# Optimization experiments

Measured on AMD Instinct MI355X. Metric: run time of the kernel, lower is better.

Reference implementation:

```python
import jax, jax.numpy as jnp
import numpy as np

N = 50000
E = 800000
G = 8
IN, HID, OUT = 128, 256, 128
BN_EPS = 1e-5


def _linear_params(key, fan_in, fan_out):
    k1, k2 = jax.random.split(key)
    s = 1.0 / np.sqrt(fan_in)
    w = jax.random.uniform(k1, (fan_out, fan_in), jnp.float32, -s, s)
    b = jax.random.uniform(k2, (fan_out,), jnp.float32, -s, s)
    return w, b


def setup_inputs() -> dict:
    key = jax.random.key(0)
    ks = jax.random.split(key, 16)
    inp = {
        "x": jax.random.normal(ks[0], (N, IN), jnp.float32),
        "src": jax.random.randint(ks[1], (E,), 0, N, jnp.int32),
        "dst": jax.random.randint(ks[2], (E,), 0, N, jnp.int32),
        "graph_ids": jnp.sort(jax.random.randint(ks[3], (N,), 0, G, jnp.int32)),
    }
    dims = [(IN, HID, HID), (HID, HID, HID), (HID, OUT, OUT)]
    for i, (d_in, d_mid, d_out) in enumerate(dims):
        kk = jax.random.split(ks[4 + i], 2)
        w1, b1 = _linear_params(kk[0], d_in, d_mid)
        w2, b2 = _linear_params(kk[1], d_mid, d_out)
        inp[f"w1_{i}"] = w1
        inp[f"b1_{i}"] = b1
        inp[f"w2_{i}"] = w2
        inp[f"b2_{i}"] = b2
        inp[f"eps_{i}"] = jnp.zeros((), jnp.float32)          # learn_eps, init 0
        inp[f"gamma_{i}"] = jnp.ones((d_out,), jnp.float32)   # BatchNorm weight
        inp[f"beta_{i}"] = jnp.zeros((d_out,), jnp.float32)   # BatchNorm bias
    return inp


def _gin_layer(h, src, dst, w1, b1, w2, b2, eps, gamma, beta):
    # GINConv: (1 + eps) * h_v + sum_{u in N(v)} h_u   (copy_u / sum)
    agg = jax.ops.segment_sum(h[src], dst, num_segments=N)
    z = (1.0 + eps) * h + agg
    # 2-layer MLP with ReLU
    z = jnp.maximum(z @ w1.T + b1, 0.0) @ w2.T + b2
    # BatchNorm1d (training-mode batch statistics, biased variance)
    mu = jnp.mean(z, axis=0)
    var = jnp.var(z, axis=0)
    return (z - mu) * jax.lax.rsqrt(var + BN_EPS) * gamma + beta


def reference(x, src, dst, graph_ids,
              w1_0, b1_0, w2_0, b2_0, eps_0, gamma_0, beta_0,
              w1_1, b1_1, w2_1, b2_1, eps_1, gamma_1, beta_1,
              w1_2, b1_2, w2_2, b2_2, eps_2, gamma_2, beta_2):
    h = _gin_layer(x, src, dst, w1_0, b1_0, w2_0, b2_0, eps_0, gamma_0, beta_0)
    h = jnp.maximum(h, 0.0)  # relu (dropout = identity in eval)
    h = _gin_layer(h, src, dst, w1_1, b1_1, w2_1, b2_1, eps_1, gamma_1, beta_1)
    h = jnp.maximum(h, 0.0)
    h = _gin_layer(h, src, dst, w1_2, b1_2, w2_2, b2_2, eps_2, gamma_2, beta_2)
    # dgl.mean_nodes: per-graph mean over nodes -> [G, OUT]
    sums = jax.ops.segment_sum(h, graph_ids, num_segments=G)
    counts = jax.ops.segment_sum(jnp.ones((N,), h.dtype), graph_ids, num_segments=G)
    return sums / jnp.maximum(counts, 1.0)[:, None]
```

## Files before the change

kernel.cpp:

```cpp
#include <hip/hip_runtime.h>

#define NG 8

typedef _Float16 half8  __attribute__((ext_vector_type(8)));
typedef float    f32x16 __attribute__((ext_vector_type(16)));


__global__ __launch_bounds__(256)
void k_cast16(const float* __restrict__ in, _Float16* __restrict__ out, int n8) {
    int i = blockIdx.x * 256 + threadIdx.x;
    if (i < n8) {
        const float4 a = *(const float4*)(in + (size_t)i * 8);
        const float4 b = *(const float4*)(in + (size_t)i * 8 + 4);
        half8 o;
        o[0] = (_Float16)a.x; o[1] = (_Float16)a.y; o[2] = (_Float16)a.z; o[3] = (_Float16)a.w;
        o[4] = (_Float16)b.x; o[5] = (_Float16)b.y; o[6] = (_Float16)b.z; o[7] = (_Float16)b.w;
        *(half8*)(out + (size_t)i * 8) = o;
    }
}


__global__ __launch_bounds__(256)
void k_deg(const int* __restrict__ dst, int* __restrict__ deg, int E) {
    int i = blockIdx.x * 256 + threadIdx.x;
    if (i < E) atomicAdd(&deg[dst[i]], 1);
}

__global__ __launch_bounds__(1024)
void k_scan_a(const int* __restrict__ deg, int* __restrict__ incl,
              int* __restrict__ bsum, int n) {
    __shared__ int s[1024];
    int t = threadIdx.x;
    int base = blockIdx.x * 1024;
    int v = (base + t < n) ? deg[base + t] : 0;
    s[t] = v;
    __syncthreads();
    for (int off = 1; off < 1024; off <<= 1) {
        int x = 0;
        if (t >= off) x = s[t - off];
        __syncthreads();
        if (t >= off) s[t] += x;
        __syncthreads();
    }
    if (base + t < n) incl[base + t] = s[t];
    if (t == 1023) bsum[blockIdx.x] = s[1023];
}

__global__ void k_scan_b(int* bsum, int nb) {
    if (threadIdx.x == 0 && blockIdx.x == 0) {
        int run = 0;
        for (int i = 0; i < nb; ++i) { int v = bsum[i]; bsum[i] = run; run += v; }
    }
}

__global__ __launch_bounds__(256)
void k_scan_c(const int* __restrict__ incl, const int* __restrict__ deg,
              const int* __restrict__ bsum, int* __restrict__ rowp, int n) {
    int i = blockIdx.x * 256 + threadIdx.x;
    if (i < n) rowp[i] = incl[i] - deg[i] + bsum[i >> 10];
}

__global__ __launch_bounds__(256)
void k_scatter(const int* __restrict__ src, const int* __restrict__ dst,
               const int* __restrict__ rowp, int* __restrict__ cur,
               int* __restrict__ ss, int E) {
    int i = blockIdx.x * 256 + threadIdx.x;
    if (i < E) {
        int d = dst[i];
        int pos = rowp[d] + atomicAdd(&cur[d], 1);
        ss[pos] = src[i];
    }
}


template<int K, bool AFFINE>
__global__ __launch_bounds__(256)
void k_agg16(const _Float16* __restrict__ h, const int* __restrict__ rowp,
             const int* __restrict__ deg, const int* __restrict__ ss,
             const float* __restrict__ eps, const float* __restrict__ scp,
             const float* __restrict__ shp, _Float16* __restrict__ z, int n) {
    constexpr int TPN = K / 8;
    constexpr int NPB = 256 / TPN;
    int node = blockIdx.x * NPB + threadIdx.x / TPN;
    int lane = threadIdx.x % TPN;
    if (node >= n) return;
    float e1 = 1.0f + eps[0];
    const int c0 = lane * 8;
    float sc[8], sh[8];
    if (AFFINE) {
#pragma unroll
        for (int e = 0; e < 8; ++e) { sc[e] = scp[c0 + e]; sh[e] = shp[c0 + e]; }
    }
    size_t base = (size_t)node * K + c0;
    half8 v = *(const half8*)(h + base);
    float a[8];
#pragma unroll
    for (int e = 0; e < 8; ++e) {
        float f = (float)v[e];
        if (AFFINE) f = fmaxf(f * sc[e] + sh[e], 0.0f);
        a[e] = f * e1;
    }
    int s  = rowp[node];
    int dn = deg[node];
    int j = 0;
    for (; j + 4 <= dn; j += 4) {
        int u0 = ss[s + j], u1 = ss[s + j + 1], u2 = ss[s + j + 2], u3 = ss[s + j + 3];
        half8 h0 = *(const half8*)(h + (size_t)u0 * K + c0);
        half8 h1 = *(const half8*)(h + (size_t)u1 * K + c0);
        half8 h2 = *(const half8*)(h + (size_t)u2 * K + c0);
        half8 h3 = *(const half8*)(h + (size_t)u3 * K + c0);
#pragma unroll
        for (int e = 0; e < 8; ++e) {
            float f0 = (float)h0[e], f1 = (float)h1[e];
            float f2 = (float)h2[e], f3 = (float)h3[e];
            if (AFFINE) {
                f0 = fmaxf(f0 * sc[e] + sh[e], 0.0f);
                f1 = fmaxf(f1 * sc[e] + sh[e], 0.0f);
                f2 = fmaxf(f2 * sc[e] + sh[e], 0.0f);
                f3 = fmaxf(f3 * sc[e] + sh[e], 0.0f);
            }
            a[e] += (f0 + f1) + (f2 + f3);
        }
    }
    for (; j < dn; ++j) {
        int u = ss[s + j];
        half8 hv = *(const half8*)(h + (size_t)u * K + c0);
#pragma unroll
        for (int e = 0; e < 8; ++e) {
            float f = (float)hv[e];
            if (AFFINE) f = fmaxf(f * sc[e] + sh[e], 0.0f);
            a[e] += f;
        }
    }
    half8 o;
#pragma unroll
    for (int e = 0; e < 8; ++e) o[e] = (_Float16)a[e];
    *(half8*)(z + base) = o;
}


template<int K, int MID, int MOUT>
__global__ __launch_bounds__(512)
void k_mlp2(const _Float16* __restrict__ A, const _Float16* __restrict__ W1,
            const float* __restrict__ b1, const _Float16* __restrict__ W2,
            const float* __restrict__ b2, _Float16* __restrict__ C,
            float* __restrict__ partial, int n) {
    constexpr int NK1 = K / 16;
    constexpr int NK2 = MID / 16;
    constexpr int NS  = K / 8;
    constexpr int MF1 = (MID == 256) ? 2 : 1;
    constexpr int MF2 = (MOUT == 256) ? 2 : 1;
    __shared__ char smem[65536];
    char* As = smem;
    char* Ys = smem + 32768;
    const int tid  = threadIdx.x;
    const int lane = tid & 63;
    const int wid  = tid >> 6;
    const int lo   = lane & 31;
    const int hi   = lane >> 5;
    const int brow = blockIdx.x * 64;

    const int wc1 = (MID == 256) ? wid : (wid & 3);
    const int wr1 = (MID == 256) ? 0   : (wid >> 2);
    const int colbase1 = wc1 * 32;
    half8 w1f[NK1];
#pragma unroll
    for (int ks = 0; ks < NK1; ++ks)
        w1f[ks] = *(const half8*)(W1 + (size_t)(colbase1 + lo) * K + ks * 16 + hi * 8);
    const float bb1 = b1[colbase1 + lo];

    {
        const int r = tid >> 3;
        int ga = brow + r; if (ga > n - 1) ga = n - 1;
        const char* Ab = (const char*)(A + (size_t)ga * K);
#pragma unroll
        for (int i = 0; i < NS / 8; ++i) {
            int l = (tid & 7) + i * 8;
            uint4 v = *(const uint4*)(Ab + l * 16);
            *(uint4*)(As + r * 512 + ((l ^ (r & 31)) << 4)) = v;
        }
    }
    __syncthreads();

    f32x16 acc1[MF1];
#pragma unroll
    for (int mf = 0; mf < MF1; ++mf)
#pragma unroll
        for (int e = 0; e < 16; ++e) acc1[mf][e] = 0.0f;

#pragma unroll
    for (int ks = 0; ks < NK1; ++ks) {
#pragma unroll
        for (int mf = 0; mf < MF1; ++mf) {
            int r = ((wr1 + mf) << 5) + lo;
            half8 af = *(const half8*)(As + r * 512 + ((ks * 32 + hi * 16) ^ ((r & 31) << 4)));
            acc1[mf] = __builtin_amdgcn_mfma_f32_32x32x16_f16(af, w1f[ks], acc1[mf], 0, 0, 0);
        }
    }

#pragma unroll
    for (int mf = 0; mf < MF1; ++mf) {
        int rb = ((wr1 + mf) << 5) + (hi << 2);
#pragma unroll
        for (int j = 0; j < 16; ++j) {
            int r = rb + (j & 3) + ((j >> 2) << 3);
            float v = fmaxf(acc1[mf][j] + bb1, 0.0f);
            *(_Float16*)(Ys + r * 512 + (((colbase1 + lo) * 2) ^ ((r & 31) << 4))) = (_Float16)v;
        }
    }

    const int wc2 = (MOUT == 256) ? wid : (wid & 3);
    const int wr2 = (MOUT == 256) ? 0   : (wid >> 2);
    const int colbase2 = wc2 * 32;
    half8 w2f[NK2];
#pragma unroll
    for (int ks = 0; ks < NK2; ++ks)
        w2f[ks] = *(const half8*)(W2 + (size_t)(colbase2 + lo) * MID + ks * 16 + hi * 8);
    const float bb2 = b2[colbase2 + lo];

    __syncthreads();

    f32x16 acc2[MF2];
#pragma unroll
    for (int mf = 0; mf < MF2; ++mf)
#pragma unroll
        for (int e = 0; e < 16; ++e) acc2[mf][e] = 0.0f;

#pragma unroll
    for (int ks = 0; ks < NK2; ++ks) {
#pragma unroll
        for (int mf = 0; mf < MF2; ++mf) {
            int r = ((wr2 + mf) << 5) + lo;
            half8 af = *(const half8*)(Ys + r * 512 + ((ks * 32 + hi * 16) ^ ((r & 31) << 4)));
            acc2[mf] = __builtin_amdgcn_mfma_f32_32x32x16_f16(af, w2f[ks], acc2[mf], 0, 0, 0);
        }
    }

    char* tb = smem + wid * 2304;
    const int g  = lane & 3;
    const int rl = lane >> 2;
    float s[8], q[8];
#pragma unroll
    for (int e = 0; e < 8; ++e) { s[e] = 0.f; q[e] = 0.f; }

#pragma unroll
    for (int mf = 0; mf < MF2; ++mf) {
#pragma unroll
        for (int j = 0; j < 16; ++j) {
            int tr = (j & 3) + ((j >> 2) << 3) + (hi << 2);
            *(_Float16*)(tb + tr * 72 + lo * 2) = (_Float16)(acc2[mf][j] + bb2);
        }
#pragma unroll
        for (int it = 0; it < 2; ++it) {
            int lr = it * 16 + rl;
            int grow = brow + ((wr2 + mf) << 5) + lr;
            half8 v = *(const half8*)(tb + lr * 72 + g * 16);
            if (grow < n) {
                *(half8*)(C + (size_t)grow * MOUT + colbase2 + g * 8) = v;
#pragma unroll
                for (int e = 0; e < 8; ++e) { float f = (float)v[e]; s[e] += f; q[e] += f * f; }
            }
        }
    }
#pragma unroll
    for (int e = 0; e < 8; ++e) {
        for (int mk = 4; mk < 64; mk <<= 1) {
            s[e] += __shfl_xor(s[e], mk, 64);
            q[e] += __shfl_xor(q[e], mk, 64);
        }
    }
    if (lane < 4) {
        float* p = partial + ((size_t)blockIdx.x * 2 + wr2) * (2 * MOUT);
#pragma unroll
        for (int e = 0; e < 8; ++e) {
            p[colbase2 + lane * 8 + e]        = s[e];
            p[MOUT + colbase2 + lane * 8 + e] = q[e];
        }
    }
}


template<int M>
__global__ __launch_bounds__(256)
void k_bnred(const float* __restrict__ partial, const float* __restrict__ gamma,
             const float* __restrict__ beta, float* __restrict__ scale,
             float* __restrict__ shift, int n, int count, int step) {
    const int w = threadIdx.x >> 6, lane = threadIdx.x & 63;
    const int c = blockIdx.x * 4 + w;
    float s = 0.f, q = 0.f;
    for (int b = lane; b < count; b += 64) {
        const float* p = partial + (size_t)(b * step) * (2 * M);
        s += p[c];
        q += p[M + c];
    }
#pragma unroll
    for (int mk = 1; mk < 64; mk <<= 1) {
        s += __shfl_xor(s, mk, 64);
        q += __shfl_xor(q, mk, 64);
    }
    if (lane == 0) {
        float invN = 1.0f / (float)n;
        float mean = s * invN;
        float var  = q * invN - mean * mean;
        float sc   = rsqrtf(var + 1e-5f) * gamma[c];
        scale[c] = sc;
        shift[c] = beta[c] - mean * sc;
    }
}


__global__ __launch_bounds__(256)
void k_readout_bn(const _Float16* __restrict__ z, const float* __restrict__ scale,
                  const float* __restrict__ shift, const int* __restrict__ gid,
                  float* __restrict__ gsum, int* __restrict__ gcnt, int n) {
    __shared__ float ls[NG * 128];
    __shared__ int   lc[NG];
    for (int i = threadIdx.x; i < NG * 128; i += 256) ls[i] = 0.0f;
    if (threadIdx.x < NG) lc[threadIdx.x] = 0;
    __syncthreads();
    int c  = threadIdx.x & 127;
    int ro = threadIdx.x >> 7;
    const float sc = scale[c];
    const float sh = shift[c];
    for (int r = blockIdx.x * 2 + ro; r < n; r += gridDim.x * 2) {
        int g = gid[r];
        float v = (float)z[(size_t)r * 128 + c] * sc + sh;
        atomicAdd(&ls[g * 128 + c], v);
        if (c == 0) atomicAdd(&lc[g], 1);
    }
    __syncthreads();
    for (int i = threadIdx.x; i < NG * 128; i += 256) atomicAdd(&gsum[i], ls[i]);
    if (threadIdx.x < NG) atomicAdd(&gcnt[threadIdx.x], lc[threadIdx.x]);
}

__global__ void k_final(const float* __restrict__ gsum, const int* __restrict__ gcnt,
                        float* __restrict__ out) {
    int i = blockIdx.x * 256 + threadIdx.x;
    if (i < NG * 128) {
        int g = i >> 7;
        out[i] = gsum[i] / fmaxf((float)gcnt[g], 1.0f);
    }
}


extern "C" void kernel_launch(void* const* d_in, const int* in_sizes, int n_in,
                              void* d_out, int out_size, void* d_ws, size_t ws_size,
                              hipStream_t stream) {
    const float* x   = (const float*)d_in[0];
    const int*   src = (const int*)d_in[1];
    const int*   dst = (const int*)d_in[2];
    const int*   gid = (const int*)d_in[3];
    const int n = in_sizes[0] / 128;
    const int E = in_sizes[1];

    auto align = [](size_t o) { return (o + 255) & ~(size_t)255; };
    char* ws = (char*)d_ws;
    size_t off = 0;
    const size_t SZ_H = align((size_t)n * 256 * sizeof(_Float16));
    const size_t SZ_I = align((size_t)n * sizeof(int));
    const int gx = (n + 63) / 64;

    _Float16* h0 = (_Float16*)(ws + off); off += align((size_t)n * 128 * sizeof(_Float16));
    _Float16* P0 = (_Float16*)(ws + off); off += SZ_H;
    _Float16* P1 = (_Float16*)(ws + off); off += SZ_H;
    int*   deg  = (int*)(ws + off);   off += SZ_I;
    int*   incl = (int*)(ws + off);   off += SZ_I;
    int*   rowp = (int*)(ws + off);   off += SZ_I;
    int*   cur  = (int*)(ws + off);   off += SZ_I;
    int*   bsum = (int*)(ws + off);   off += 256 * sizeof(int);
    int*   ss   = (int*)(ws + off);   off += align((size_t)E * sizeof(int));
    float* partial = (float*)(ws + off); off += align((size_t)gx * 2 * 2 * 256 * sizeof(float));
    float* scale   = (float*)(ws + off); off += align(256 * sizeof(float));
    float* shiftb  = (float*)(ws + off); off += align(256 * sizeof(float));
    float* gsum = (float*)(ws + off); off += align(NG * 128 * sizeof(float));
    int*   gcnt = (int*)(ws + off);   off += align(NG * sizeof(int));
    _Float16* wh[6];
    for (int i = 0; i < 6; ++i) { wh[i] = (_Float16*)(ws + off); off += align(65536 * sizeof(_Float16)); }

    const int Ks[3]    = {128, 256, 256};
    const int Mids[3]  = {256, 256, 128};
    const int Mouts[3] = {256, 256, 128};

    k_cast16<<<(n * 128 / 8 + 255) / 256, 256, 0, stream>>>(x, h0, n * 128 / 8);
    for (int L = 0; L < 3; ++L) {
        const int base = 4 + 7 * L;
        int n1 = Mids[L] * Ks[L];
        int n2 = Mouts[L] * Mids[L];
        k_cast16<<<(n1 / 8 + 255) / 256, 256, 0, stream>>>((const float*)d_in[base + 0], wh[2 * L + 0], n1 / 8);
        k_cast16<<<(n2 / 8 + 255) / 256, 256, 0, stream>>>((const float*)d_in[base + 2], wh[2 * L + 1], n2 / 8);
    }

    hipMemsetAsync(deg, 0, (size_t)n * sizeof(int), stream);
    k_deg<<<(E + 255) / 256, 256, 0, stream>>>(dst, deg, E);
    int nb = (n + 1023) / 1024;
    k_scan_a<<<nb, 1024, 0, stream>>>(deg, incl, bsum, n);
    k_scan_b<<<1, 1, 0, stream>>>(bsum, nb);
    k_scan_c<<<(n + 255) / 256, 256, 0, stream>>>(incl, deg, bsum, rowp, n);
    hipMemsetAsync(cur, 0, (size_t)n * sizeof(int), stream);
    k_scatter<<<(E + 255) / 256, 256, 0, stream>>>(src, dst, rowp, cur, ss, E);

    for (int L = 0; L < 3; ++L) {
        const int base = 4 + 7 * L;
        const float* b1    = (const float*)d_in[base + 1];
        const float* b2    = (const float*)d_in[base + 3];
        const float* eps   = (const float*)d_in[base + 4];
        const float* gamma = (const float*)d_in[base + 5];
        const float* beta  = (const float*)d_in[base + 6];

        if (L == 0) {
            k_agg16<128, false><<<(n + 15) / 16, 256, 0, stream>>>(
                h0, rowp, deg, ss, eps, nullptr, nullptr, P1, n);
            k_mlp2<128, 256, 256><<<gx, 512, 0, stream>>>(P1, wh[0], b1, wh[1], b2, P0, partial, n);
            k_bnred<256><<<64, 256, 0, stream>>>(partial, gamma, beta, scale, shiftb, n, gx, 2);
        } else if (L == 1) {
            k_agg16<256, true><<<(n + 7) / 8, 256, 0, stream>>>(
                P0, rowp, deg, ss, eps, scale, shiftb, P1, n);
            k_mlp2<256, 256, 256><<<gx, 512, 0, stream>>>(P1, wh[2], b1, wh[3], b2, P0, partial, n);
            k_bnred<256><<<64, 256, 0, stream>>>(partial, gamma, beta, scale, shiftb, n, gx, 2);
        } else {
            k_agg16<256, true><<<(n + 7) / 8, 256, 0, stream>>>(
                P0, rowp, deg, ss, eps, scale, shiftb, P1, n);
            k_mlp2<256, 128, 128><<<gx, 512, 0, stream>>>(P1, wh[4], b1, wh[5], b2, P0, partial, n);
            k_bnred<128><<<32, 256, 0, stream>>>(partial, gamma, beta, scale, shiftb, n, 2 * gx, 1);
        }
    }

    hipMemsetAsync(gsum, 0, NG * 128 * sizeof(float), stream);
    hipMemsetAsync(gcnt, 0, NG * sizeof(int), stream);
    k_readout_bn<<<256, 256, 0, stream>>>(P0, scale, shiftb, gid, gsum, gcnt, n);
    k_final<<<4, 256, 0, stream>>>(gsum, gcnt, (float*)d_out);
}
```

Measured before the change: 438.4 us.

## Make MLP kernel persistent with register-prefetched tiles and batch weight casts

The fused two-layer MLP kernel becomes persistent: 256 blocks loop over 64-row tiles. Both weight fragment sets are loaded into registers once per block, and the next tile's activations are prefetched into registers while the current tile computes. BN partial sums are accumulated across tiles, so the reduction reads 256 blocks' partials instead of one per tile. The six weight-cast launches are merged into one kernel. The aim is to remove repeated weight loads and launch overhead and to hide global-load latency, at the cost of higher register pressure and possibly lower occupancy.

```diff
diff --git a/kernel.cpp b/kernel.cpp
--- a/kernel.cpp
+++ b/kernel.cpp
@@ -17,6 +17,31 @@
         o[4] = (_Float16)b.x; o[5] = (_Float16)b.y; o[6] = (_Float16)b.z; o[7] = (_Float16)b.w;
         *(half8*)(out + (size_t)i * 8) = o;
     }
+}
+
+__global__ __launch_bounds__(256)
+void k_castw(const float* __restrict__ w0, const float* __restrict__ w1,
+             const float* __restrict__ w2, const float* __restrict__ w3,
+             const float* __restrict__ w4, const float* __restrict__ w5,
+             _Float16* __restrict__ o0, _Float16* __restrict__ o1,
+             _Float16* __restrict__ o2, _Float16* __restrict__ o3,
+             _Float16* __restrict__ o4, _Float16* __restrict__ o5) {
+    int i = blockIdx.x * 256 + threadIdx.x;
+    const float* in; _Float16* out; int off;
+    if      (i <  4096) { in = w0; out = o0; off = 0;     }
+    else if (i < 12288) { in = w1; out = o1; off = 4096;  }
+    else if (i < 20480) { in = w2; out = o2; off = 12288; }
+    else if (i < 28672) { in = w3; out = o3; off = 20480; }
+    else if (i < 32768) { in = w4; out = o4; off = 28672; }
+    else if (i < 34816) { in = w5; out = o5; off = 32768; }
+    else return;
+    int j = i - off;
+    const float4 a = *(const float4*)(in + (size_t)j * 8);
+    const float4 b = *(const float4*)(in + (size_t)j * 8 + 4);
+    half8 o;
+    o[0] = (_Float16)a.x; o[1] = (_Float16)a.y; o[2] = (_Float16)a.z; o[3] = (_Float16)a.w;
+    o[4] = (_Float16)b.x; o[5] = (_Float16)b.y; o[6] = (_Float16)b.z; o[7] = (_Float16)b.w;
+    *(half8*)(out + (size_t)j * 8) = o;
 }
 
 
@@ -141,127 +166,137 @@
 
 template<int K, int MID, int MOUT>
 __global__ __launch_bounds__(512)
-void k_mlp2(const _Float16* __restrict__ A, const _Float16* __restrict__ W1,
+void k_mlp3(const _Float16* __restrict__ A, const _Float16* __restrict__ W1,
             const float* __restrict__ b1, const _Float16* __restrict__ W2,
             const float* __restrict__ b2, _Float16* __restrict__ C,
-            float* __restrict__ partial, int n) {
+            float* __restrict__ partial, int n, int ntiles) {
     constexpr int NK1 = K / 16;
     constexpr int NK2 = MID / 16;
-    constexpr int NS  = K / 8;
     constexpr int MF1 = (MID == 256) ? 2 : 1;
     constexpr int MF2 = (MOUT == 256) ? 2 : 1;
-    __shared__ char smem[65536];
-    char* As = smem;
-    char* Ys = smem + 32768;
+    constexpr int NLD = K / 64;
+    __shared__ char As[64 * 512];
+    __shared__ char Ys[64 * 512];
+    __shared__ char tbs[8 * 2304];
     const int tid  = threadIdx.x;
     const int lane = tid & 63;
     const int wid  = tid >> 6;
     const int lo   = lane & 31;
     const int hi   = lane >> 5;
-    const int brow = blockIdx.x * 64;
 
     const int wc1 = (MID == 256) ? wid : (wid & 3);
     const int wr1 = (MID == 256) ? 0   : (wid >> 2);
     const int colbase1 = wc1 * 32;
-    half8 w1f[NK1];
-#pragma unroll
-    for (int ks = 0; ks < NK1; ++ks)
-        w1f[ks] = *(const half8*)(W1 + (size_t)(colbase1 + lo) * K + ks * 16 + hi * 8);
-    const float bb1 = b1[colbase1 + lo];
-
-    {
-        const int r = tid >> 3;
-        int ga = brow + r; if (ga > n - 1) ga = n - 1;
-        const char* Ab = (const char*)(A + (size_t)ga * K);
-#pragma unroll
-        for (int i = 0; i < NS / 8; ++i) {
-            int l = (tid & 7) + i * 8;
-            uint4 v = *(const uint4*)(Ab + l * 16);
-            *(uint4*)(As + r * 512 + ((l ^ (r & 31)) << 4)) = v;
-        }
-    }
-    __syncthreads();
-
-    f32x16 acc1[MF1];
-#pragma unroll
-    for (int mf = 0; mf < MF1; ++mf)
-#pragma unroll
-        for (int e = 0; e < 16; ++e) acc1[mf][e] = 0.0f;
-
-#pragma unroll
-    for (int ks = 0; ks < NK1; ++ks) {
-#pragma unroll
-        for (int mf = 0; mf < MF1; ++mf) {
-            int r = ((wr1 + mf) << 5) + lo;
-            half8 af = *(const half8*)(As + r * 512 + ((ks * 32 + hi * 16) ^ ((r & 31) << 4)));
-            acc1[mf] = __builtin_amdgcn_mfma_f32_32x32x16_f16(af, w1f[ks], acc1[mf], 0, 0, 0);
-        }
-    }
-
-#pragma unroll
-    for (int mf = 0; mf < MF1; ++mf) {
-        int rb = ((wr1 + mf) << 5) + (hi << 2);
-#pragma unroll
-        for (int j = 0; j < 16; ++j) {
-            int r = rb + (j & 3) + ((j >> 2) << 3);
-            float v = fmaxf(acc1[mf][j] + bb1, 0.0f);
-            *(_Float16*)(Ys + r * 512 + (((colbase1 + lo) * 2) ^ ((r & 31) << 4))) = (_Float16)v;
-        }
-    }
-
     const int wc2 = (MOUT == 256) ? wid : (wid & 3);
     const int wr2 = (MOUT == 256) ? 0   : (wid >> 2);
     const int colbase2 = wc2 * 32;
-    half8 w2f[NK2];
+
+    half8 w1f[NK1], w2f[NK2];
+#pragma unroll
+    for (int ks = 0; ks < NK1; ++ks)
+        w1f[ks] = *(const half8*)(W1 + (size_t)(colbase1 + lo) * K + ks * 16 + hi * 8);
 #pragma unroll
     for (int ks = 0; ks < NK2; ++ks)
         w2f[ks] = *(const half8*)(W2 + (size_t)(colbase2 + lo) * MID + ks * 16 + hi * 8);
+    const float bb1 = b1[colbase1 + lo];
     const float bb2 = b2[colbase2 + lo];
 
-    __syncthreads();
-
-    f32x16 acc2[MF2];
-#pragma unroll
-    for (int mf = 0; mf < MF2; ++mf)
-#pragma unroll
-        for (int e = 0; e < 16; ++e) acc2[mf][e] = 0.0f;
-
-#pragma unroll
-    for (int ks = 0; ks < NK2; ++ks) {
-#pragma unroll
-        for (int mf = 0; mf < MF2; ++mf) {
-            int r = ((wr2 + mf) << 5) + lo;
-            half8 af = *(const half8*)(Ys + r * 512 + ((ks * 32 + hi * 16) ^ ((r & 31) << 4)));
-            acc2[mf] = __builtin_amdgcn_mfma_f32_32x32x16_f16(af, w2f[ks], acc2[mf], 0, 0, 0);
-        }
-    }
-
-    char* tb = smem + wid * 2304;
+    const int sr = tid >> 3;
+    const int sl = tid & 7;
     const int g  = lane & 3;
     const int rl = lane >> 2;
+    char* tb = tbs + wid * 2304;
+
     float s[8], q[8];
 #pragma unroll
     for (int e = 0; e < 8; ++e) { s[e] = 0.f; q[e] = 0.f; }
 
-#pragma unroll
-    for (int mf = 0; mf < MF2; ++mf) {
-#pragma unroll
-        for (int j = 0; j < 16; ++j) {
-            int tr = (j & 3) + ((j >> 2) << 3) + (hi << 2);
-            *(_Float16*)(tb + tr * 72 + lo * 2) = (_Float16)(acc2[mf][j] + bb2);
-        }
-#pragma unroll
-        for (int it = 0; it < 2; ++it) {
-            int lr = it * 16 + rl;
-            int grow = brow + ((wr2 + mf) << 5) + lr;
-            half8 v = *(const half8*)(tb + lr * 72 + g * 16);
-            if (grow < n) {
-                *(half8*)(C + (size_t)grow * MOUT + colbase2 + g * 8) = v;
-#pragma unroll
-                for (int e = 0; e < 8; ++e) { float f = (float)v[e]; s[e] += f; q[e] += f * f; }
-            }
-        }
-    }
+    int tile = blockIdx.x;
+    uint4 ar[NLD];
+    if (tile < ntiles) {
+        int ga = tile * 64 + sr; if (ga > n - 1) ga = n - 1;
+        const char* Ab = (const char*)(A + (size_t)ga * K);
+#pragma unroll
+        for (int i = 0; i < NLD; ++i) ar[i] = *(const uint4*)(Ab + (sl + i * 8) * 16);
+    }
+
+    for (; tile < ntiles; tile += gridDim.x) {
+        const int brow = tile * 64;
+
+#pragma unroll
+        for (int i = 0; i < NLD; ++i)
+            *(uint4*)(As + sr * 512 + (((sl + i * 8) ^ (sr & 31)) << 4)) = ar[i];
+        int nt = tile + gridDim.x;
+        if (nt < ntiles) {
+            int ga = nt * 64 + sr; if (ga > n - 1) ga = n - 1;
+            const char* Ab = (const char*)(A + (size_t)ga * K);
+#pragma unroll
+            for (int i = 0; i < NLD; ++i) ar[i] = *(const uint4*)(Ab + (sl + i * 8) * 16);
+        }
+        __syncthreads();
+
+        f32x16 acc1[MF1];
+#pragma unroll
+        for (int mf = 0; mf < MF1; ++mf)
+#pragma unroll
+            for (int e = 0; e < 16; ++e) acc1[mf][e] = 0.0f;
+#pragma unroll
+        for (int ks = 0; ks < NK1; ++ks) {
+#pragma unroll
+            for (int mf = 0; mf < MF1; ++mf) {
+                int r = ((wr1 + mf) << 5) + lo;
+                half8 af = *(const half8*)(As + r * 512 + ((ks * 32 + hi * 16) ^ ((r & 31) << 4)));
+                acc1[mf] = __builtin_amdgcn_mfma_f32_32x32x16_f16(af, w1f[ks], acc1[mf], 0, 0, 0);
+            }
+        }
+#pragma unroll
+        for (int mf = 0; mf < MF1; ++mf) {
+            int rb = ((wr1 + mf) << 5) + (hi << 2);
+#pragma unroll
+            for (int j = 0; j < 16; ++j) {
+                int r = rb + (j & 3) + ((j >> 2) << 3);
+                float v = fmaxf(acc1[mf][j] + bb1, 0.0f);
+                *(_Float16*)(Ys + r * 512 + (((colbase1 + lo) * 2) ^ ((r & 31) << 4))) = (_Float16)v;
+            }
+        }
+        __syncthreads();
+
+        f32x16 acc2[MF2];
+#pragma unroll
+        for (int mf = 0; mf < MF2; ++mf)
+#pragma unroll
+            for (int e = 0; e < 16; ++e) acc2[mf][e] = 0.0f;
+#pragma unroll
+        for (int ks = 0; ks < NK2; ++ks) {
+#pragma unroll
+            for (int mf = 0; mf < MF2; ++mf) {
+                int r = ((wr2 + mf) << 5) + lo;
+                half8 af = *(const half8*)(Ys + r * 512 + ((ks * 32 + hi * 16) ^ ((r & 31) << 4)));
+                acc2[mf] = __builtin_amdgcn_mfma_f32_32x32x16_f16(af, w2f[ks], acc2[mf], 0, 0, 0);
+            }
+        }
+
+#pragma unroll
+        for (int mf = 0; mf < MF2; ++mf) {
+#pragma unroll
+            for (int j = 0; j < 16; ++j) {
+                int tr = (j & 3) + ((j >> 2) << 3) + (hi << 2);
+                *(_Float16*)(tb + tr * 72 + lo * 2) = (_Float16)(acc2[mf][j] + bb2);
+            }
+#pragma unroll
+            for (int it = 0; it < 2; ++it) {
+                int lr = it * 16 + rl;
+                int grow = brow + ((wr2 + mf) << 5) + lr;
+                half8 v = *(const half8*)(tb + lr * 72 + g * 16);
+                if (grow < n) {
+                    *(half8*)(C + (size_t)grow * MOUT + colbase2 + g * 8) = v;
+#pragma unroll
+                    for (int e = 0; e < 8; ++e) { float f = (float)v[e]; s[e] += f; q[e] += f * f; }
+                }
+            }
+        }
+    }
+
 #pragma unroll
     for (int e = 0; e < 8; ++e) {
         for (int mk = 4; mk < 64; mk <<= 1) {
@@ -359,6 +394,7 @@
     const size_t SZ_H = align((size_t)n * 256 * sizeof(_Float16));
     const size_t SZ_I = align((size_t)n * sizeof(int));
     const int gx = (n + 63) / 64;
+    const int NBLK = 256;
 
     _Float16* h0 = (_Float16*)(ws + off); off += align((size_t)n * 128 * sizeof(_Float16));
     _Float16* P0 = (_Float16*)(ws + off); off += SZ_H;
@@ -369,7 +405,7 @@
     int*   cur  = (int*)(ws + off);   off += SZ_I;
     int*   bsum = (int*)(ws + off);   off += 256 * sizeof(int);
     int*   ss   = (int*)(ws + off);   off += align((size_t)E * sizeof(int));
-    float* partial = (float*)(ws + off); off += align((size_t)gx * 2 * 2 * 256 * sizeof(float));
+    float* partial = (float*)(ws + off); off += align((size_t)(2 * NBLK) * 2 * 256 * sizeof(float));
     float* scale   = (float*)(ws + off); off += align(256 * sizeof(float));
     float* shiftb  = (float*)(ws + off); off += align(256 * sizeof(float));
     float* gsum = (float*)(ws + off); off += align(NG * 128 * sizeof(float));
@@ -377,18 +413,12 @@
     _Float16* wh[6];
     for (int i = 0; i < 6; ++i) { wh[i] = (_Float16*)(ws + off); off += align(65536 * sizeof(_Float16)); }
 
-    const int Ks[3]    = {128, 256, 256};
-    const int Mids[3]  = {256, 256, 128};
-    const int Mouts[3] = {256, 256, 128};
-
     k_cast16<<<(n * 128 / 8 + 255) / 256, 256, 0, stream>>>(x, h0, n * 128 / 8);
-    for (int L = 0; L < 3; ++L) {
-        const int base = 4 + 7 * L;
-        int n1 = Mids[L] * Ks[L];
-        int n2 = Mouts[L] * Mids[L];
-        k_cast16<<<(n1 / 8 + 255) / 256, 256, 0, stream>>>((const float*)d_in[base + 0], wh[2 * L + 0], n1 / 8);
-        k_cast16<<<(n2 / 8 + 255) / 256, 256, 0, stream>>>((const float*)d_in[base + 2], wh[2 * L + 1], n2 / 8);
-    }
+    k_castw<<<136, 256, 0, stream>>>(
+        (const float*)d_in[4], (const float*)d_in[6],
+        (const float*)d_in[11], (const float*)d_in[13],
+        (const float*)d_in[18], (const float*)d_in[20],
+        wh[0], wh[1], wh[2], wh[3], wh[4], wh[5]);
 
     hipMemsetAsync(deg, 0, (size_t)n * sizeof(int), stream);
     k_deg<<<(E + 255) / 256, 256, 0, stream>>>(dst, deg, E);
@@ -410,18 +440,18 @@
         if (L == 0) {
             k_agg16<128, false><<<(n + 15) / 16, 256, 0, stream>>>(
                 h0, rowp, deg, ss, eps, nullptr, nullptr, P1, n);
-            k_mlp2<128, 256, 256><<<gx, 512, 0, stream>>>(P1, wh[0], b1, wh[1], b2, P0, partial, n);
-            k_bnred<256><<<64, 256, 0, stream>>>(partial, gamma, beta, scale, shiftb, n, gx, 2);
+            k_mlp3<128, 256, 256><<<NBLK, 512, 0, stream>>>(P1, wh[0], b1, wh[1], b2, P0, partial, n, gx);
+            k_bnred<256><<<64, 256, 0, stream>>>(partial, gamma, beta, scale, shiftb, n, NBLK, 2);
         } else if (L == 1) {
             k_agg16<256, true><<<(n + 7) / 8, 256, 0, stream>>>(
                 P0, rowp, deg, ss, eps, scale, shiftb, P1, n);
-            k_mlp2<256, 256, 256><<<gx, 512, 0, stream>>>(P1, wh[2], b1, wh[3], b2, P0, partial, n);
-            k_bnred<256><<<64, 256, 0, stream>>>(partial, gamma, beta, scale, shiftb, n, gx, 2);
+            k_mlp3<256, 256, 256><<<NBLK, 512, 0, stream>>>(P1, wh[2], b1, wh[3], b2, P0, partial, n, gx);
+            k_bnred<256><<<64, 256, 0, stream>>>(partial, gamma, beta, scale, shiftb, n, NBLK, 2);
         } else {
             k_agg16<256, true><<<(n + 7) / 8, 256, 0, stream>>>(
                 P0, rowp, deg, ss, eps, scale, shiftb, P1, n);
-            k_mlp2<256, 128, 128><<<gx, 512, 0, stream>>>(P1, wh[4], b1, wh[5], b2, P0, partial, n);
-            k_bnred<128><<<32, 256, 0, stream>>>(partial, gamma, beta, scale, shiftb, n, 2 * gx, 1);
+            k_mlp3<256, 128, 128><<<NBLK, 512, 0, stream>>>(P1, wh[4], b1, wh[5], b2, P0, partial, n, gx);
+            k_bnred<128><<<32, 256, 0, stream>>>(partial, gamma, beta, scale, shiftb, n, 2 * NBLK, 1);
         }
     }
 
```

Measured after the change: 411.5 us. -6.1%, faster.
